# Kernel tuning notes

Measured on AMD Instinct MI355X. Metric: run time of the kernel, lower is better.

Reference implementation:

```python
import math
import jax, jax.numpy as jnp
import numpy as np

B, S, F, I, K, L, C = 2, 2048, 512, 1024, 3, 2, 256
BETA = 0.99                 # momentumnet_beta
INIT_SCALE = L ** -0.5      # per-cell output scale
PI = math.pi


def setup_inputs() -> dict:
    key = jax.random.key(0)
    ks = jax.random.split(key, 8)
    inp = jax.random.randint(ks[0], (B, S), 0, C)
    tgt = jax.random.randint(ks[1], (B, S), 0, C)
    emb = jax.random.normal(ks[2], (C, 2 * F), jnp.float32) * 0.02
    w0s = jax.random.normal(ks[3], (L, 3, I, F, 1), jnp.float32) * (F ** -0.5)
    w1s = jax.random.normal(ks[4], (L, 3, I, I, K), jnp.float32) * ((I * K) ** -0.5)
    w2s = jax.random.normal(ks[5], (L, 3, F, I, 1), jnp.float32) * (I ** -0.5)
    out_w = jax.random.normal(ks[6], (C, 2 * F, 1), jnp.float32) * ((2 * F) ** -0.5)
    out_b = jax.random.normal(ks[7], (C,), jnp.float32) * 0.02
    return {"inp": inp, "tgt": tgt, "emb": emb, "w0s": w0s, "w1s": w1s,
            "w2s": w2s, "out_w": out_w, "out_b": out_b}


def causal_conv(x, w):
    # x: [B, Cin, S], w: [Cout, Cin, k]; left-pad k-1 (matches torch pad+(k-1,0)+conv1d)
    k = w.shape[-1]
    return jax.lax.conv_general_dilated(x, w, (1,), [(k - 1, 0)],
                                        dimension_numbers=("NCH", "OIH", "NCH"))


def feed_forward(x, w0, w1, w2):
    x = jax.nn.relu(causal_conv(x, w0))
    x = jax.nn.relu(causal_conv(x, w1))
    return causal_conv(x, w2)


def norm(x):
    # mean-subtract + RMS-style L2 norm over channel dim (dim 1)
    x = x - x.mean(1, keepdims=True)
    return x / (jnp.linalg.norm(x, axis=1, keepdims=True) * (x.shape[1] ** -0.5) + 1e-5)


def _feature_embd():
    f = jnp.arange(F, dtype=jnp.float32)[:, None] + 1.0
    additive = f % 2.0
    f = (f - additive) / 2.0
    f = f * (8.0 / F) - math.log(C / (2.0 * PI))
    return jnp.exp(f) + additive * PI  # [F, 1]


def _forward(inp, tgt, emb, w0s, w1s, w2s, out_w, out_b):
    fe = _feature_embd()
    divisor = (jnp.arange(S, dtype=jnp.float32) + 1.0)[None, None, :]  # [1,1,S]
    x = emb[inp].transpose(0, 2, 1)         # [B, 2F, S]
    a, b = x[:, :F], x[:, F:]               # reversible streams [B, F, S]
    for l in range(L):
        h = b + fe                          # training-path positional embedding
        d = feed_forward(h, w0s[l, 0], w1s[l, 0], w2s[l, 0])
        sc = feed_forward(h, w0s[l, 1], w1s[l, 1], w2s[l, 1])
        sh = feed_forward(h, w0s[l, 2], w1s[l, 2], w2s[l, 2])
        cum = jnp.cumsum(d, axis=1)         # cumsum over feature dim (dim 1, as in source)
        cell = norm(cum / divisor * sc + sh) * INIT_SCALE
        c = BETA * a + (1.0 - BETA) * cell  # momentum coupling forward
        a, b = c, b + c                     # Identity layer with additive coupling
    streams = jnp.concatenate([a, b], axis=1)        # [B, 2F, S]
    logits = causal_conv(streams, out_w) + out_b[None, :, None]  # [B, C, S]
    logp = jax.nn.log_softmax(logits, axis=1)
    nll = -jnp.take_along_axis(logp, tgt[:, None, :], axis=1)[:, 0, :]
    return nll.mean()                       # torch cross_entropy (mean reduction)


def reference(inp, tgt, emb, w0s, w1s, w2s, out_w, out_b):
    return _forward(inp, tgt, emb, w0s, w1s, w2s, out_w, out_b)
```

## Files before the change

### kernel.cpp

```cpp
#include <hip/hip_runtime.h>

#define S_ 2048
#define F_ 512
#define I_ 1024
#define C_ 256

typedef float f4 __attribute__((ext_vector_type(4)));
typedef __bf16 bf8 __attribute__((ext_vector_type(8)));
typedef __bf16 bf4 __attribute__((ext_vector_type(4)));
typedef int i4v __attribute__((ext_vector_type(4)));
typedef int i8v __attribute__((ext_vector_type(8)));
typedef unsigned char u8;

__device__ __forceinline__ void gload_lds16(const void* g, void* l) {
  __builtin_amdgcn_global_load_lds(
      (const __attribute__((address_space(1))) void*)g,
      (__attribute__((address_space(3))) void*)l, 16, 0, 0);
}

__device__ __forceinline__ float fe_val(int f) {
  const float PI_F = 3.14159265358979323846f;
  float additive = (f & 1) ? 0.0f : 1.0f;
  float fv = ((float)(f + 1) - additive) * 0.5f;
  fv = fv * (8.0f / (float)F_) - logf((float)C_ / (2.0f * PI_F));
  return expf(fv) + additive * PI_F;
}

template <int KW, bool RELU, int OUT, int NTILE, int KD, int LDB>
__global__ __launch_bounds__(256, 3) void gemm_f8(
    const u8* __restrict__ Ab, const u8* __restrict__ Bb, void* __restrict__ Cb,
    const u8* __restrict__ zpage, int M, int PZ, long sAp, long sBp, long sBb,
    long sCz) {
  constexpr int NF = NTILE / 32;
  constexpr int NIT = KD / 128;
  constexpr int AK = KW * KD;
  constexpr int BP = NTILE / 32;
  constexpr int NSTEP = KW * NIT;
  constexpr int LOG_NIT = (NIT == 4) ? 2 : 3;
  static_assert(NIT == (1 << LOG_NIT), "NIT pow2");
  static_assert(NSTEP % 2 == 0, "even k-step count required");
  __shared__ u8 Asm[128 * 128];
  __shared__ u8 Bsm[2][NTILE * 128];
  const int tid = threadIdx.x;
  const int z = blockIdx.z;
  const int p = z % PZ;
  const int bb = z / PZ;
  const u8* A = Ab + (long)p * sAp;
  const u8* B = Bb + (long)bb * sBb + (long)p * sBp;
  const int m0 = blockIdx.y * 128;
  const int n0 = blockIdx.x * NTILE;
  const int lane = tid & 63;
  const int wave = tid >> 6;
  const int wr = wave >> 1;
  const int wc = wave & 1;
  const int l15 = lane & 15;
  const int quad = lane >> 4;
  const int cr = tid >> 3;
  const int csw = (((tid & 7) ^ (cr & 7)) << 4);
  const int off0 = (((2 * quad) ^ (l15 & 7)) << 4);
  const int off1 = (((2 * quad + 1) ^ (l15 & 7)) << 4);
  f4 acc[4][NF] = {};

  const u8* pA0 = A + (long)(m0 + cr) * AK + csw;
  const int rb0 = n0 + cr + ((KW == 3) ? -2 : 0);
  const u8* pB0 = B + (long)rb0 * LDB + csw;
  const u8* zpc = zpage + csw;

  auto stageA = [&](int ks) {
    const int uoff = ((ks >> LOG_NIT) * KD) + ((ks & (NIT - 1)) << 7);
#pragma unroll
    for (int g = 0; g < 4; ++g)
      gload_lds16(pA0 + (long)(g * 32) * AK + uoff,
                  Asm + g * 4096 + wave * 1024);
  };

  auto stageB = [&](int ks, int buf) {
    const int t = ks >> LOG_NIT;
    const int uoff = t * LDB + ((ks & (NIT - 1)) << 7);
#pragma unroll
    for (int g = 0; g < BP; ++g) {
      const u8* src = pB0 + (long)(g * 32) * LDB + uoff;
      if (KW == 3 && (rb0 + g * 32 + t) < 0) src = zpc;
      gload_lds16(src, &Bsm[buf][g * 4096 + wave * 1024]);
    }
  };

  auto compute = [&](int buf) {
    i8v af[4], bfr[NF];
#pragma unroll
    for (int mt = 0; mt < 4; ++mt) {
      const u8* rp = Asm + (wr * 64 + mt * 16 + l15) * 128;
      const i4v lo = *(const i4v*)(rp + off0);
      const i4v hi = *(const i4v*)(rp + off1);
      af[mt][0] = lo[0]; af[mt][1] = lo[1]; af[mt][2] = lo[2]; af[mt][3] = lo[3];
      af[mt][4] = hi[0]; af[mt][5] = hi[1]; af[mt][6] = hi[2]; af[mt][7] = hi[3];
    }
#pragma unroll
    for (int nt = 0; nt < NF; ++nt) {
      const u8* rp = &Bsm[buf][(wc * (NTILE / 2) + nt * 16 + l15) * 128];
      const i4v lo = *(const i4v*)(rp + off0);
      const i4v hi = *(const i4v*)(rp + off1);
      bfr[nt][0] = lo[0]; bfr[nt][1] = lo[1]; bfr[nt][2] = lo[2]; bfr[nt][3] = lo[3];
      bfr[nt][4] = hi[0]; bfr[nt][5] = hi[1]; bfr[nt][6] = hi[2]; bfr[nt][7] = hi[3];
    }
#pragma unroll
    for (int mt = 0; mt < 4; ++mt)
#pragma unroll
      for (int nt = 0; nt < NF; ++nt)
        acc[mt][nt] = __builtin_amdgcn_mfma_scale_f32_16x16x128_f8f6f4(
            af[mt], bfr[nt], acc[mt][nt], 0, 0, 0, 0x7F7F7F7F, 0, 0x7F7F7F7F);
  };

  stageA(0);
  stageB(0, 0);
  __syncthreads();
#pragma unroll 1
  for (int ks = 0; ks < NSTEP; ks += 2) {
    stageB(ks + 1, 1);
    compute(0);
    __syncthreads();
    stageA(ks + 1);
    __syncthreads();
    if (ks + 2 < NSTEP) stageB(ks + 2, 0);
    compute(1);
    __syncthreads();
    if (ks + 2 < NSTEP) {
      stageA(ks + 2);
      __syncthreads();
    }
  }

#pragma unroll
  for (int mt = 0; mt < 4; ++mt) {
    const int m = m0 + wr * 64 + mt * 16 + quad * 4;
#pragma unroll
    for (int nt = 0; nt < NF; ++nt) {
      const int n = n0 + wc * (NTILE / 2) + nt * 16 + l15;
      f4 v = acc[mt][nt];
#pragma unroll
      for (int q = 0; q < 4; ++q) {
        v[q] *= 0.015625f;
        if (RELU) v[q] = fmaxf(v[q], 0.0f);
      }
      if (OUT == 2) {
        int r = __builtin_amdgcn_cvt_pk_fp8_f32(v[0], v[1], 0, false);
        r = __builtin_amdgcn_cvt_pk_fp8_f32(v[2], v[3], r, true);
        *(int*)((u8*)Cb + (long)z * sCz + (long)n * M + m) = r;
      } else {
        *(f4*)((float*)Cb + (long)z * sCz + (long)n * M + m) = v;
      }
    }
  }
}

__device__ __forceinline__ void cvt4(const float* __restrict__ s,
                                     __bf16* __restrict__ d, long T) {
  const long i = T * 4;
  const float4 v = *(const float4*)(s + i);
  bf4 o;
  o[0] = (__bf16)v.x;
  o[1] = (__bf16)v.y;
  o[2] = (__bf16)v.z;
  o[3] = (__bf16)v.w;
  *(bf4*)(d + i) = o;
}

__device__ __forceinline__ void cvt4f8(const float* __restrict__ s,
                                       u8* __restrict__ d, long T) {
  const long i = T * 4;
  const float4 v = *(const float4*)(s + i);
  int r = __builtin_amdgcn_cvt_pk_fp8_f32(v.x * 64.0f, v.y * 64.0f, 0, false);
  r = __builtin_amdgcn_cvt_pk_fp8_f32(v.z * 64.0f, v.w * 64.0f, r, true);
  *(int*)(d + i) = r;
}

__device__ __forceinline__ int pk4f8(float a, float b, float c, float d) {
  int r = __builtin_amdgcn_cvt_pk_fp8_f32(a, b, 0, false);
  return __builtin_amdgcn_cvt_pk_fp8_f32(c, d, r, true);
}

__global__ void k_prep(const float* __restrict__ w0, const float* __restrict__ w2,
                       const float* __restrict__ ow, const float* __restrict__ w1,
                       u8* __restrict__ W0f8, u8* __restrict__ W2f8,
                       __bf16* __restrict__ OWc, u8* __restrict__ W1f8) {
  long T = (long)blockIdx.x * 256 + threadIdx.x;
  if (T < 786432L) {
    cvt4f8(w0, W0f8, T);
    return;
  }
  T -= 786432L;
  if (T < 786432L) {
    cvt4f8(w2, W2f8, T);
    return;
  }
  T -= 786432L;
  if (T < 65536L) {
    cvt4(ow, OWc, T);
    return;
  }
  T -= 65536L;
  const long j4 = T & 255;
  const long r3 = T >> 8;
  const float* src = w1 + r3 * 3072 + j4 * 12;
  const float4 v0 = *(const float4*)src;
  const float4 v1 = *(const float4*)(src + 4);
  const float4 v2 = *(const float4*)(src + 8);
  u8* dst = W1f8 + r3 * 3072 + j4 * 4;
  *(int*)(dst) = pk4f8(v0.x * 64.f, v0.w * 64.f, v1.z * 64.f, v2.y * 64.f);
  *(int*)(dst + 1024) = pk4f8(v0.y * 64.f, v1.x * 64.f, v1.w * 64.f, v2.z * 64.f);
  *(int*)(dst + 2048) = pk4f8(v0.z * 64.f, v1.y * 64.f, v2.x * 64.f, v2.w * 64.f);
}

__global__ __launch_bounds__(64) void k_embed(const int* __restrict__ inp,
                                              const float* __restrict__ emb,
                                              float* __restrict__ a_st,
                                              float* __restrict__ b_st,
                                              u8* __restrict__ h) {
  const int col = blockIdx.x;
  const int lane = threadIdx.x;
  const int f0 = lane * 8;
  const float* e = emb + (long)inp[col] * (2 * F_);
  const float4 a0 = *(const float4*)(e + f0);
  const float4 a1 = *(const float4*)(e + f0 + 4);
  const float4 b0 = *(const float4*)(e + F_ + f0);
  const float4 b1 = *(const float4*)(e + F_ + f0 + 4);
  *(float4*)(a_st + (long)col * F_ + f0) = a0;
  *(float4*)(a_st + (long)col * F_ + f0 + 4) = a1;
  *(float4*)(b_st + (long)col * F_ + f0) = b0;
  *(float4*)(b_st + (long)col * F_ + f0 + 4) = b1;
  const float bb[8] = {b0.x, b0.y, b0.z, b0.w, b1.x, b1.y, b1.z, b1.w};
  float hv[8];
#pragma unroll
  for (int q = 0; q < 8; ++q) hv[q] = bb[q] + fe_val(f0 + q);
  const int lo = pk4f8(hv[0], hv[1], hv[2], hv[3]);
  const int hi = pk4f8(hv[4], hv[5], hv[6], hv[7]);
  *(int2*)(h + (long)col * F_ + f0) = {lo, hi};
}

__global__ __launch_bounds__(64) void k_cell(const float* __restrict__ Y3,
                                             float* __restrict__ a_st,
                                             float* __restrict__ b_st,
                                             void* __restrict__ outp,
                                             int last) {
  const int col = blockIdx.x;
  const int s = col & (S_ - 1);
  const int b = col >> 11;
  const int lane = threadIdx.x;
  const int f0 = lane * 8;
  const float* d = Y3 + ((long)(3 * b + 0) * S_ + s) * F_ + f0;
  const float* sc = Y3 + ((long)(3 * b + 1) * S_ + s) * F_ + f0;
  const float* sh = Y3 + ((long)(3 * b + 2) * S_ + s) * F_ + f0;
  float* ap = a_st + (long)col * F_ + f0;
  float* bp = b_st + (long)col * F_ + f0;
  const float inv_div = 1.0f / (float)(s + 1);

  const float4 d0 = *(const float4*)d;
  const float4 d1 = *(const float4*)(d + 4);
  const float4 sc0 = *(const float4*)sc;
  const float4 sc1 = *(const float4*)(sc + 4);
  const float4 sh0 = *(const float4*)sh;
  const float4 sh1 = *(const float4*)(sh + 4);

  float c[8];
  c[0] = d0.x;
  c[1] = c[0] + d0.y;
  c[2] = c[1] + d0.z;
  c[3] = c[2] + d0.w;
  c[4] = c[3] + d1.x;
  c[5] = c[4] + d1.y;
  c[6] = c[5] + d1.z;
  c[7] = c[6] + d1.w;
  const float tot = c[7];
  float scan = tot;
#pragma unroll
  for (int off = 1; off < 64; off <<= 1) {
    float nb = __shfl_up(scan, off);
    if (lane >= off) scan += nb;
  }
  const float base = scan - tot;

  float v[8];
  v[0] = (base + c[0]) * inv_div * sc0.x + sh0.x;
  v[1] = (base + c[1]) * inv_div * sc0.y + sh0.y;
  v[2] = (base + c[2]) * inv_div * sc0.z + sh0.z;
  v[3] = (base + c[3]) * inv_div * sc0.w + sh0.w;
  v[4] = (base + c[4]) * inv_div * sc1.x + sh1.x;
  v[5] = (base + c[5]) * inv_div * sc1.y + sh1.y;
  v[6] = (base + c[6]) * inv_div * sc1.z + sh1.z;
  v[7] = (base + c[7]) * inv_div * sc1.w + sh1.w;

  float sum = 0.f, ssq = 0.f;
#pragma unroll
  for (int q = 0; q < 8; ++q) {
    sum += v[q];
    ssq += v[q] * v[q];
  }
#pragma unroll
  for (int off = 1; off < 64; off <<= 1) {
    sum += __shfl_xor(sum, off);
    ssq += __shfl_xor(ssq, off);
  }
  const float mean = sum * (1.0f / (float)F_);
  const float nsq = fmaxf(ssq - (float)F_ * mean * mean, 0.0f);
  const float denom = sqrtf(nsq) * 0.04419417382415922f + 1e-5f;
  const float isc = 0.7071067811865476f / denom;

  const float4 av0 = *(const float4*)ap;
  const float4 av1 = *(const float4*)(ap + 4);
  const float4 bv0 = *(const float4*)bp;
  const float4 bv1 = *(const float4*)(bp + 4);
  float an[8], bn[8];
  const float ai[8] = {av0.x, av0.y, av0.z, av0.w, av1.x, av1.y, av1.z, av1.w};
  const float bi[8] = {bv0.x, bv0.y, bv0.z, bv0.w, bv1.x, bv1.y, bv1.z, bv1.w};
#pragma unroll
  for (int q = 0; q < 8; ++q) {
    const float cell = (v[q] - mean) * isc;
    an[q] = 0.99f * ai[q] + 0.01f * cell;
    bn[q] = bi[q] + an[q];
  }
  *(float4*)ap = {an[0], an[1], an[2], an[3]};
  *(float4*)(ap + 4) = {an[4], an[5], an[6], an[7]};
  *(float4*)bp = {bn[0], bn[1], bn[2], bn[3]};
  *(float4*)(bp + 4) = {bn[4], bn[5], bn[6], bn[7]};
  if (!last) {
    float hv[8];
#pragma unroll
    for (int q = 0; q < 8; ++q) hv[q] = bn[q] + fe_val(f0 + q);
    const int lo = pk4f8(hv[0], hv[1], hv[2], hv[3]);
    const int hi = pk4f8(hv[4], hv[5], hv[6], hv[7]);
    *(int2*)((u8*)outp + (long)col * F_ + f0) = {lo, hi};
  } else {
    bf8 oa, ob;
#pragma unroll
    for (int q = 0; q < 8; ++q) {
      oa[q] = (__bf16)an[q];
      ob[q] = (__bf16)bn[q];
    }
    *(bf8*)((__bf16*)outp + (long)col * (2 * F_) + f0) = oa;
    *(bf8*)((__bf16*)outp + (long)col * (2 * F_) + F_ + f0) = ob;
  }
}

__global__ __launch_bounds__(256) void k_logits_nll(
    const __bf16* __restrict__ A, const __bf16* __restrict__ Bb,
    const float* __restrict__ outb, const int* __restrict__ tgt,
    float* __restrict__ acc) {
  __shared__ __bf16 As[256 * 32];
  __shared__ __bf16 Bs[32 * 32];
  __shared__ float lsm[32 * 256];
  const int tid = threadIdx.x;
  const int b = blockIdx.y;
  const int n0 = blockIdx.x * 32;
  const __bf16* Bt = Bb + (long)b * (S_ * 2 * F_) + (long)n0 * (2 * F_);
  const int lane = tid & 63;
  const int wave = tid >> 6;
  const int l15 = lane & 15;
  const int quad = lane >> 4;
  const int cr = tid >> 2;
  const int csw = (((tid & 3) ^ ((cr >> 1) & 3)) << 3);
  const int roff = ((quad ^ ((l15 >> 1) & 3)) << 3);
  f4 av[4][2] = {};
  for (int k0 = 0; k0 < 2 * F_; k0 += 32) {
#pragma unroll
    for (int i = 0; i < 4; ++i)
      gload_lds16(A + (long)(i * 64 + cr) * (2 * F_) + (k0 + csw),
                  As + ((i * 256 + (wave << 6)) << 3));
    if (wave < 2)
      gload_lds16(Bt + (long)cr * (2 * F_) + (k0 + csw),
                  Bs + ((wave << 6) << 3));
    __syncthreads();
    bf8 af[4], bfr[2];
#pragma unroll
    for (int mt = 0; mt < 4; ++mt)
      af[mt] = *(const bf8*)(As + (wave * 64 + mt * 16 + l15) * 32 + roff);
#pragma unroll
    for (int nt = 0; nt < 2; ++nt)
      bfr[nt] = *(const bf8*)(Bs + (nt * 16 + l15) * 32 + roff);
#pragma unroll
    for (int mt = 0; mt < 4; ++mt)
#pragma unroll
      for (int nt = 0; nt < 2; ++nt)
        av[mt][nt] = __builtin_amdgcn_mfma_f32_16x16x32_bf16(af[mt], bfr[nt],
                                                             av[mt][nt], 0, 0, 0);
    __syncthreads();
  }
#pragma unroll
  for (int mt = 0; mt < 4; ++mt) {
    const int m = wave * 64 + mt * 16 + quad * 4;
#pragma unroll
    for (int nt = 0; nt < 2; ++nt) {
      const int pp = nt * 16 + l15;
      *(f4*)(lsm + pp * C_ + m) = av[mt][nt];
    }
  }
  __syncthreads();
  const float4 bv = *(const float4*)(outb + lane * 4);
  float wsum = 0.f;
  for (int i = 0; i < 8; ++i) {
    const int pp = wave * 8 + i;
    const f4 lv = *(const f4*)(lsm + pp * C_ + lane * 4);
    const float x0 = lv[0] + bv.x, x1 = lv[1] + bv.y, x2 = lv[2] + bv.z,
                x3 = lv[3] + bv.w;
    float mx = fmaxf(fmaxf(x0, x1), fmaxf(x2, x3));
#pragma unroll
    for (int off = 1; off < 64; off <<= 1) mx = fmaxf(mx, __shfl_xor(mx, off));
    float ss = expf(x0 - mx) + expf(x1 - mx) + expf(x2 - mx) + expf(x3 - mx);
#pragma unroll
    for (int off = 1; off < 64; off <<= 1) ss += __shfl_xor(ss, off);
    if (lane == 0) {
      const int t = tgt[b * S_ + n0 + pp];
      wsum += mx + logf(ss) - (lsm[pp * C_ + t] + outb[t]);
    }
  }
  if (lane == 0) atomicAdd(acc, wsum);
}

__global__ void k_final(const float* __restrict__ acc, float* __restrict__ out) {
  out[0] = acc[0] * (1.0f / 4096.0f);
}

extern "C" void kernel_launch(void* const* d_in, const int* in_sizes, int n_in,
                              void* d_out, int out_size, void* d_ws,
                              size_t ws_size, hipStream_t stream) {
  const int* inp = (const int*)d_in[0];
  const int* tgt = (const int*)d_in[1];
  const float* emb = (const float*)d_in[2];
  const float* w0s = (const float*)d_in[3];
  const float* w1s = (const float*)d_in[4];
  const float* w2s = (const float*)d_in[5];
  const float* out_w = (const float*)d_in[6];
  const float* out_b = (const float*)d_in[7];

  char* ws = (char*)d_ws;
  float* acc = (float*)(ws + 0);
  u8* zp = (u8*)(ws + 256);
  float* a_st = (float*)(ws + 4096);
  float* b_st = (float*)(ws + 8392704L);
  u8* h = (u8*)(ws + 16781312L);
  u8* Y1f8 = (u8*)(ws + 20975616L);
  u8* Y2f8 = (u8*)(ws + 46141440L);
  float* Y3 = (float*)(ws + 71307264L);
  u8* W1f8 = (u8*)(ws + 96473088L);
  __bf16* streams = (__bf16*)(ws + 134221824L);
  u8* W0f8 = (u8*)(ws + 146804736L);
  u8* W2f8 = (u8*)(ws + 153096192L);
  __bf16* OWc = (__bf16*)(ws + 159387648L);

  hipMemsetAsync(ws, 0, 4096, stream);
  k_prep<<<12544, 256, 0, stream>>>(w0s, w2s, out_w, w1s, W0f8, W2f8, OWc, W1f8);
  k_embed<<<4096, 64, 0, stream>>>(inp, emb, a_st, b_st, h);

  for (int l = 0; l < 2; ++l) {
    gemm_f8<1, true, 2, 128, 512, 512><<<dim3(16, 24, 2), 256, 0, stream>>>(
        W0f8 + (long)l * 1572864L, h, Y1f8, zp, 3072, 1, 0L, 0L, 1048576L,
        6291456L);
    gemm_f8<3, true, 2, 128, 1024, 3072><<<dim3(16, 8, 6), 256, 0, stream>>>(
        W1f8 + (long)l * 9437184L, Y1f8, Y2f8, zp, 1024, 3, 3145728L, 1024L,
        6291456L, 2097152L);
    gemm_f8<1, false, 0, 64, 1024, 1024><<<dim3(32, 4, 6), 256, 0, stream>>>(
        W2f8 + (long)l * 1572864L, Y2f8, Y3, zp, 512, 3, 524288L, 2097152L,
        6291456L, 1048576L);
    k_cell<<<4096, 64, 0, stream>>>(Y3, a_st, b_st,
                                    (l == 0) ? (void*)h : (void*)streams,
                                    (l == 1) ? 1 : 0);
  }

  k_logits_nll<<<dim3(64, 2), 256, 0, stream>>>(OWc, streams, out_b, tgt, acc);
  k_final<<<1, 1, 0, stream>>>(acc, (float*)d_out);
}
```

Measured before the change: 360.1 us.

## Fuse embed and workspace zeroing into prep, fold final into logits kernel

Merges the embedding gather and the workspace memset into the k_prep launch, and replaces the separate k_final kernel with a last-block-done counter inside k_logits_nll. k_cell now packs four columns per 256-thread block, and the logits kernel halves its column tile to 16 so twice as many blocks run. The aim is to cut launch count and per-launch overhead and to raise occupancy in the small kernels. The cost is a grid-wide atomic counter completion pattern and a smaller MFMA tile with less reuse of A in the logits GEMM.

Measured after the change: 357.5 us. No clear change (-0.7%).

```diff
diff --git a/kernel.cpp b/kernel.cpp
--- a/kernel.cpp
+++ b/kernel.cpp
@@ -182,8 +182,40 @@
 __global__ void k_prep(const float* __restrict__ w0, const float* __restrict__ w2,
                        const float* __restrict__ ow, const float* __restrict__ w1,
                        u8* __restrict__ W0f8, u8* __restrict__ W2f8,
-                       __bf16* __restrict__ OWc, u8* __restrict__ W1f8) {
-  long T = (long)blockIdx.x * 256 + threadIdx.x;
+                       __bf16* __restrict__ OWc, u8* __restrict__ W1f8,
+                       const int* __restrict__ inp, const float* __restrict__ emb,
+                       float* __restrict__ a_st, float* __restrict__ b_st,
+                       u8* __restrict__ h, int* __restrict__ wsz) {
+  const int bx = blockIdx.x;
+  const int tid = threadIdx.x;
+  if (bx >= 13568) {
+    i4v zv = {0, 0, 0, 0};
+    *(i4v*)((u8*)wsz + tid * 16) = zv;
+    return;
+  }
+  if (bx >= 12544) {
+    const int col = ((bx - 12544) << 2) + (tid >> 6);
+    const int lane = tid & 63;
+    const int f0 = lane * 8;
+    const float* e = emb + (long)inp[col] * (2 * F_);
+    const float4 a0 = *(const float4*)(e + f0);
+    const float4 a1 = *(const float4*)(e + f0 + 4);
+    const float4 b0 = *(const float4*)(e + F_ + f0);
+    const float4 b1 = *(const float4*)(e + F_ + f0 + 4);
+    *(float4*)(a_st + (long)col * F_ + f0) = a0;
+    *(float4*)(a_st + (long)col * F_ + f0 + 4) = a1;
+    *(float4*)(b_st + (long)col * F_ + f0) = b0;
+    *(float4*)(b_st + (long)col * F_ + f0 + 4) = b1;
+    const float bb[8] = {b0.x, b0.y, b0.z, b0.w, b1.x, b1.y, b1.z, b1.w};
+    float hv[8];
+#pragma unroll
+    for (int q = 0; q < 8; ++q) hv[q] = bb[q] + fe_val(f0 + q);
+    const int lo = pk4f8(hv[0], hv[1], hv[2], hv[3]);
+    const int hi = pk4f8(hv[4], hv[5], hv[6], hv[7]);
+    *(int2*)(h + (long)col * F_ + f0) = {lo, hi};
+    return;
+  }
+  long T = (long)bx * 256 + tid;
   if (T < 786432L) {
     cvt4f8(w0, W0f8, T);
     return;
@@ -211,41 +243,15 @@
   *(int*)(dst + 2048) = pk4f8(v0.z * 64.f, v1.y * 64.f, v2.x * 64.f, v2.w * 64.f);
 }
 
-__global__ __launch_bounds__(64) void k_embed(const int* __restrict__ inp,
-                                              const float* __restrict__ emb,
+__global__ __launch_bounds__(256) void k_cell(const float* __restrict__ Y3,
                                               float* __restrict__ a_st,
                                               float* __restrict__ b_st,
-                                              u8* __restrict__ h) {
-  const int col = blockIdx.x;
-  const int lane = threadIdx.x;
-  const int f0 = lane * 8;
-  const float* e = emb + (long)inp[col] * (2 * F_);
-  const float4 a0 = *(const float4*)(e + f0);
-  const float4 a1 = *(const float4*)(e + f0 + 4);
-  const float4 b0 = *(const float4*)(e + F_ + f0);
-  const float4 b1 = *(const float4*)(e + F_ + f0 + 4);
-  *(float4*)(a_st + (long)col * F_ + f0) = a0;
-  *(float4*)(a_st + (long)col * F_ + f0 + 4) = a1;
-  *(float4*)(b_st + (long)col * F_ + f0) = b0;
-  *(float4*)(b_st + (long)col * F_ + f0 + 4) = b1;
-  const float bb[8] = {b0.x, b0.y, b0.z, b0.w, b1.x, b1.y, b1.z, b1.w};
-  float hv[8];
-#pragma unroll
-  for (int q = 0; q < 8; ++q) hv[q] = bb[q] + fe_val(f0 + q);
-  const int lo = pk4f8(hv[0], hv[1], hv[2], hv[3]);
-  const int hi = pk4f8(hv[4], hv[5], hv[6], hv[7]);
-  *(int2*)(h + (long)col * F_ + f0) = {lo, hi};
-}
-
-__global__ __launch_bounds__(64) void k_cell(const float* __restrict__ Y3,
-                                             float* __restrict__ a_st,
-                                             float* __restrict__ b_st,
-                                             void* __restrict__ outp,
-                                             int last) {
-  const int col = blockIdx.x;
+                                              void* __restrict__ outp,
+                                              int last) {
+  const int col = (blockIdx.x << 2) + (threadIdx.x >> 6);
   const int s = col & (S_ - 1);
   const int b = col >> 11;
-  const int lane = threadIdx.x;
+  const int lane = threadIdx.x & 63;
   const int f0 = lane * 8;
   const float* d = Y3 + ((long)(3 * b + 0) * S_ + s) * F_ + f0;
   const float* sc = Y3 + ((long)(3 * b + 1) * S_ + s) * F_ + f0;
@@ -344,13 +350,14 @@
 __global__ __launch_bounds__(256) void k_logits_nll(
     const __bf16* __restrict__ A, const __bf16* __restrict__ Bb,
     const float* __restrict__ outb, const int* __restrict__ tgt,
-    float* __restrict__ acc) {
+    float* __restrict__ acc, unsigned* __restrict__ cnt,
+    float* __restrict__ out) {
   __shared__ __bf16 As[256 * 32];
-  __shared__ __bf16 Bs[32 * 32];
-  __shared__ float lsm[32 * 256];
+  __shared__ __bf16 Bs[16 * 32];
+  __shared__ float lsm[16 * 256];
   const int tid = threadIdx.x;
   const int b = blockIdx.y;
-  const int n0 = blockIdx.x * 32;
+  const int n0 = blockIdx.x * 16;
   const __bf16* Bt = Bb + (long)b * (S_ * 2 * F_) + (long)n0 * (2 * F_);
   const int lane = tid & 63;
   const int wave = tid >> 6;
@@ -359,45 +366,36 @@
   const int cr = tid >> 2;
   const int csw = (((tid & 3) ^ ((cr >> 1) & 3)) << 3);
   const int roff = ((quad ^ ((l15 >> 1) & 3)) << 3);
-  f4 av[4][2] = {};
+  f4 av[4] = {};
   for (int k0 = 0; k0 < 2 * F_; k0 += 32) {
 #pragma unroll
     for (int i = 0; i < 4; ++i)
       gload_lds16(A + (long)(i * 64 + cr) * (2 * F_) + (k0 + csw),
                   As + ((i * 256 + (wave << 6)) << 3));
-    if (wave < 2)
-      gload_lds16(Bt + (long)cr * (2 * F_) + (k0 + csw),
-                  Bs + ((wave << 6) << 3));
+    if (wave == 0)
+      gload_lds16(Bt + (long)cr * (2 * F_) + (k0 + csw), Bs);
     __syncthreads();
-    bf8 af[4], bfr[2];
+    bf8 af[4], bf0;
 #pragma unroll
     for (int mt = 0; mt < 4; ++mt)
       af[mt] = *(const bf8*)(As + (wave * 64 + mt * 16 + l15) * 32 + roff);
-#pragma unroll
-    for (int nt = 0; nt < 2; ++nt)
-      bfr[nt] = *(const bf8*)(Bs + (nt * 16 + l15) * 32 + roff);
+    bf0 = *(const bf8*)(Bs + (l15)*32 + roff);
 #pragma unroll
     for (int mt = 0; mt < 4; ++mt)
-#pragma unroll
-      for (int nt = 0; nt < 2; ++nt)
-        av[mt][nt] = __builtin_amdgcn_mfma_f32_16x16x32_bf16(af[mt], bfr[nt],
-                                                             av[mt][nt], 0, 0, 0);
+      av[mt] = __builtin_amdgcn_mfma_f32_16x16x32_bf16(af[mt], bf0, av[mt], 0,
+                                                       0, 0);
     __syncthreads();
   }
 #pragma unroll
   for (int mt = 0; mt < 4; ++mt) {
     const int m = wave * 64 + mt * 16 + quad * 4;
-#pragma unroll
-    for (int nt = 0; nt < 2; ++nt) {
-      const int pp = nt * 16 + l15;
-      *(f4*)(lsm + pp * C_ + m) = av[mt][nt];
-    }
+    *(f4*)(lsm + l15 * C_ + m) = av[mt];
   }
   __syncthreads();
   const float4 bv = *(const float4*)(outb + lane * 4);
   float wsum = 0.f;
-  for (int i = 0; i < 8; ++i) {
-    const int pp = wave * 8 + i;
+  for (int i = 0; i < 4; ++i) {
+    const int pp = wave * 4 + i;
     const f4 lv = *(const f4*)(lsm + pp * C_ + lane * 4);
     const float x0 = lv[0] + bv.x, x1 = lv[1] + bv.y, x2 = lv[2] + bv.z,
                 x3 = lv[3] + bv.w;
@@ -413,10 +411,15 @@
     }
   }
   if (lane == 0) atomicAdd(acc, wsum);
-}
-
-__global__ void k_final(const float* __restrict__ acc, float* __restrict__ out) {
-  out[0] = acc[0] * (1.0f / 4096.0f);
+  __syncthreads();
+  if (tid == 0) {
+    const unsigned nblk = gridDim.x * gridDim.y;
+    const unsigned old = atomicAdd(cnt, 1u);
+    if (old == nblk - 1) {
+      const float v = atomicAdd(acc, 0.0f);
+      out[0] = v * (1.0f / 4096.0f);
+    }
+  }
 }
 
 extern "C" void kernel_launch(void* const* d_in, const int* in_sizes, int n_in,
@@ -433,6 +436,7 @@
 
   char* ws = (char*)d_ws;
   float* acc = (float*)(ws + 0);
+  unsigned* cnt = (unsigned*)(ws + 16);
   u8* zp = (u8*)(ws + 256);
   float* a_st = (float*)(ws + 4096);
   float* b_st = (float*)(ws + 8392704L);
@@ -446,9 +450,8 @@
   u8* W2f8 = (u8*)(ws + 153096192L);
   __bf16* OWc = (__bf16*)(ws + 159387648L);
 
-  hipMemsetAsync(ws, 0, 4096, stream);
-  k_prep<<<12544, 256, 0, stream>>>(w0s, w2s, out_w, w1s, W0f8, W2f8, OWc, W1f8);
-  k_embed<<<4096, 64, 0, stream>>>(inp, emb, a_st, b_st, h);
+  k_prep<<<13569, 256, 0, stream>>>(w0s, w2s, out_w, w1s, W0f8, W2f8, OWc,
+                                    W1f8, inp, emb, a_st, b_st, h, (int*)ws);
 
   for (int l = 0; l < 2; ++l) {
     gemm_f8<1, true, 2, 128, 512, 512><<<dim3(16, 24, 2), 256, 0, stream>>>(
@@ -460,11 +463,11 @@
     gemm_f8<1, false, 0, 64, 1024, 1024><<<dim3(32, 4, 6), 256, 0, stream>>>(
         W2f8 + (long)l * 1572864L, Y2f8, Y3, zp, 512, 3, 524288L, 2097152L,
         6291456L, 1048576L);
-    k_cell<<<4096, 64, 0, stream>>>(Y3, a_st, b_st,
-                                    (l == 0) ? (void*)h : (void*)streams,
-                                    (l == 1) ? 1 : 0);
-  }
-
-  k_logits_nll<<<dim3(64, 2), 256, 0, stream>>>(OWc, streams, out_b, tgt, acc);
-  k_final<<<1, 1, 0, stream>>>(acc, (float*)d_out);
-}
+    k_cell<<<1024, 256, 0, stream>>>(Y3, a_st, b_st,
+                                     (l == 0) ? (void*)h : (void*)streams,
+                                     (l == 1) ? 1 : 0);
+  }
+
+  k_logits_nll<<<dim3(128, 2), 256, 0, stream>>>(OWc, streams, out_b, tgt, acc,
+                                                 cnt, (float*)d_out);
+}
```
